# Optimization experiments

Hardware: AMD Instinct MI355X
Metric: run time of the kernel (lower is better)

Reference implementation:

```python
import jax, jax.numpy as jnp
import numpy as np

LN_EPS = 1e-5  # torch.nn.LayerNorm default


def setup_inputs() -> dict:
    key = jax.random.key(0)
    k1, k2, k3 = jax.random.split(key, 3)
    B, N, F, D = 8, 2048, 128, 128
    A_hat = jax.random.uniform(k1, (B, N, N), dtype=jnp.float32)
    X = jax.random.normal(k2, (B, N, F), dtype=jnp.float32)
    W = jax.random.normal(k3, (D, F), dtype=jnp.float32) * (1.0 / np.sqrt(F))
    b = jnp.zeros((D,), dtype=jnp.float32)
    gamma = jnp.ones((D,), dtype=jnp.float32)
    beta = jnp.zeros((D,), dtype=jnp.float32)
    return {"A_hat": A_hat, "X": X, "W": W, "b": b, "gamma": gamma, "beta": beta}


def reference(A_hat, X, W, b, gamma, beta):
    # batched aggregation: H[b] = A_hat[b] @ X[b]   (torch loop over batch, vectorized here)
    H = jnp.einsum('bnm,bmf->bnf', A_hat, X)
    # linear: torch nn.Linear stores W as [out, in]
    H = jnp.einsum('bnf,df->bnd', H, W) + b
    # LayerNorm over last dim, then ReLU (dropout p=0 -> identity)
    mu = jnp.mean(H, axis=-1, keepdims=True)
    var = jnp.mean((H - mu) ** 2, axis=-1, keepdims=True)
    Hn = (H - mu) * jax.lax.rsqrt(var + LN_EPS) * gamma + beta
    return jax.nn.relu(Hn)
```

## Files before the change

### kernel.cpp

```cpp
#include <hip/hip_runtime.h>
#include <stdint.h>

#define B_DIM 8
#define N_DIM 2048
#define F_DIM 128
#define LN_EPS 1e-5f

typedef __attribute__((ext_vector_type(8))) short short8;
typedef __attribute__((ext_vector_type(4))) float floatx4;

__device__ __forceinline__ ushort f2bf(float f) {
    union { float f; uint32_t u; } c;
    c.f = f;
    uint32_t u = c.u;
    return (ushort)((u + 0x7FFFu + ((u >> 16) & 1u)) >> 16);
}

__device__ __forceinline__ uint32_t pk2bf(float a, float b) {
    union { float f; uint32_t u; } x, y;
    x.f = a; y.f = b;
    return ((x.u + 0x8000u) >> 16) | ((y.u + 0x8000u) & 0xFFFF0000u);
}

__device__ __forceinline__ short8 pack8(float4 lo, float4 hi) {
    union { uint32_t u[4]; short8 s; } r;
    r.u[0] = pk2bf(lo.x, lo.y);
    r.u[1] = pk2bf(lo.z, lo.w);
    r.u[2] = pk2bf(hi.x, hi.y);
    r.u[3] = pk2bf(hi.z, hi.w);
    return r.s;
}

__device__ __forceinline__ void load_lds16(const ushort* g, ushort* l) {
    __builtin_amdgcn_global_load_lds(
        (const __attribute__((address_space(1))) void*)g,
        (__attribute__((address_space(3))) void*)l,
        16, 0, 0);
}

__global__ __launch_bounds__(256) void k_transpose(const float* __restrict__ X,
                                                   ushort* __restrict__ Xt) {
    __shared__ ushort tile[64 * 65];
    const int t = threadIdx.x;
    const int b = blockIdx.z;
    const int k0 = blockIdx.x * 64;
    const int f0 = blockIdx.y * 64;

#pragma unroll
    for (int p = 0; p < 2; ++p) {
        int idx = p * 256 + t;
        int kk = idx >> 3;
        int ff = (idx & 7) * 8;
        const float* src = X + (((size_t)b * N_DIM) + k0 + kk) * F_DIM + f0 + ff;
        float4 v0 = *(const float4*)(src);
        float4 v1 = *(const float4*)(src + 4);
        ushort* d = tile + kk * 65 + ff;
        d[0] = f2bf(v0.x); d[1] = f2bf(v0.y); d[2] = f2bf(v0.z); d[3] = f2bf(v0.w);
        d[4] = f2bf(v1.x); d[5] = f2bf(v1.y); d[6] = f2bf(v1.z); d[7] = f2bf(v1.w);
    }
    __syncthreads();

    union U { uint4 v; ushort s[8]; };
#pragma unroll
    for (int p = 0; p < 2; ++p) {
        int idx = p * 256 + t;
        int f2 = idx >> 3;
        int kk2 = (idx & 7) * 8;
        U u;
#pragma unroll
        for (int j = 0; j < 8; ++j) u.s[j] = tile[(kk2 + j) * 65 + f2];
        *(uint4*)(Xt + (((size_t)b * F_DIM) + f0 + f2) * N_DIM + k0 + kk2) = u.v;
    }
}

__global__ __launch_bounds__(256) void k_fused(const float* __restrict__ A,
                                               const ushort* __restrict__ Xt,
                                               const float* __restrict__ W,
                                               const float* __restrict__ bias,
                                               const float* __restrict__ gamma,
                                               const float* __restrict__ beta,
                                               float* __restrict__ out) {
    __shared__ __align__(16) ushort As[32 * 128];
    __shared__ __align__(16) ushort Bs[128 * 128];
    __shared__ __align__(16) ushort Ht[32 * 136];
    __shared__ float Pt[32][132];

    const int t = threadIdx.x;
    const int lane = t & 63;
    const int w = t >> 6;
    const int q = lane >> 4;
    const int mr = lane & 15;

    const int bid = blockIdx.x;
    const int bb = bid & 7;
    const int m0 = (bid >> 3) * 32;

    const float* Ab = A + ((size_t)bb * N_DIM + m0) * N_DIM;
    const ushort* Xb = Xt + (size_t)bb * F_DIM * N_DIM;

    const int arow = t >> 3;
    const int asw_ = arow & 7;
    const float* a_src = Ab + (size_t)arow * N_DIM + (t & 7) * 16;
    ushort* a_dst0 = As + arow * 128 + ((((t & 7) * 2) ^ asw_) * 8);
    ushort* a_dst1 = As + arow * 128 + ((((t & 7) * 2 + 1) ^ asw_) * 8);

    const ushort* b_src[8];
    ushort* b_dst[8];
#pragma unroll
    for (int p = 0; p < 8; ++p) {
        int c = p * 256 + t;
        int n = c >> 4;
        int kc = (c & 15) ^ (n & 7);
        b_src[p] = Xb + (size_t)n * N_DIM + kc * 8;
        b_dst[p] = Bs + c * 8;
    }

    floatx4 acc[2][2];
#pragma unroll
    for (int i = 0; i < 2; ++i)
#pragma unroll
        for (int j = 0; j < 2; ++j) acc[i][j] = (floatx4){0.f, 0.f, 0.f, 0.f};

    for (int k0 = 0; k0 < N_DIM; k0 += 128) {
        float4 v0 = ((const float4*)(a_src + k0))[0];
        float4 v1 = ((const float4*)(a_src + k0))[1];
        float4 v2 = ((const float4*)(a_src + k0))[2];
        float4 v3 = ((const float4*)(a_src + k0))[3];
#pragma unroll
        for (int p = 0; p < 8; ++p) load_lds16(b_src[p] + k0, b_dst[p]);
        *(short8*)a_dst0 = pack8(v0, v1);
        *(short8*)a_dst1 = pack8(v2, v3);
        __syncthreads();

#pragma unroll
        for (int ks = 0; ks < 4; ++ks) {
            short8 af[2], bf[2];
#pragma unroll
            for (int i = 0; i < 2; ++i) {
                int m = mr + i * 16;
                af[i] = *(const short8*)(As + m * 128 + (((ks * 4 + q) ^ (m & 7)) * 8));
            }
#pragma unroll
            for (int j = 0; j < 2; ++j) {
                int n = w * 32 + j * 16 + mr;
                bf[j] = *(const short8*)(Bs + n * 128 + (((ks * 4 + q) ^ (n & 7)) * 8));
            }
#pragma unroll
            for (int i = 0; i < 2; ++i)
#pragma unroll
                for (int j = 0; j < 2; ++j)
                    acc[i][j] = __builtin_amdgcn_mfma_f32_16x16x32_bf16(
                        af[i], bf[j], acc[i][j], 0, 0, 0);
        }
        __syncthreads();
    }

#pragma unroll
    for (int j = 0; j < 2; ++j) {
        int col = w * 32 + j * 16 + mr;
#pragma unroll
        for (int r = 0; r < 4; ++r) {
            Ht[(q * 4 + r) * 136 + col] = f2bf(acc[0][j][r]);
            Ht[(16 + q * 4 + r) * 136 + col] = f2bf(acc[1][j][r]);
        }
    }
    __syncthreads();

    floatx4 p[2][2];
#pragma unroll
    for (int i = 0; i < 2; ++i)
#pragma unroll
        for (int j = 0; j < 2; ++j) p[i][j] = (floatx4){0.f, 0.f, 0.f, 0.f};

#pragma unroll
    for (int ks = 0; ks < 4; ++ks) {
        short8 ha0 = *(const short8*)(Ht + mr * 136 + ks * 32 + q * 8);
        short8 ha1 = *(const short8*)(Ht + (mr + 16) * 136 + ks * 32 + q * 8);
#pragma unroll
        for (int j = 0; j < 2; ++j) {
            const float* wp = W + (w * 32 + j * 16 + mr) * F_DIM + ks * 32 + q * 8;
            short8 wb = pack8(((const float4*)wp)[0], ((const float4*)wp)[1]);
            p[0][j] = __builtin_amdgcn_mfma_f32_16x16x32_bf16(ha0, wb, p[0][j], 0, 0, 0);
            p[1][j] = __builtin_amdgcn_mfma_f32_16x16x32_bf16(ha1, wb, p[1][j], 0, 0, 0);
        }
    }

#pragma unroll
    for (int j = 0; j < 2; ++j) {
        int col = w * 32 + j * 16 + mr;
        float bcol = bias[col];
#pragma unroll
        for (int r = 0; r < 4; ++r) {
            Pt[q * 4 + r][col] = p[0][j][r] + bcol;
            Pt[16 + q * 4 + r][col] = p[1][j][r] + bcol;
        }
    }
    __syncthreads();

    const int row = t >> 3;
    const int seg = t & 7;
    float v[16];
    float s = 0.f, s2 = 0.f;
#pragma unroll
    for (int u = 0; u < 16; ++u) {
        v[u] = Pt[row][seg * 16 + u];
        s += v[u];
        s2 += v[u] * v[u];
    }
    s += __shfl_xor(s, 1);  s2 += __shfl_xor(s2, 1);
    s += __shfl_xor(s, 2);  s2 += __shfl_xor(s2, 2);
    s += __shfl_xor(s, 4);  s2 += __shfl_xor(s2, 4);
    float mu = s * (1.0f / 128.0f);
    float var = s2 * (1.0f / 128.0f) - mu * mu;
    float rs = rsqrtf(var + LN_EPS);

    float4 o[4];
    float* of = (float*)o;
#pragma unroll
    for (int u = 0; u < 16; ++u) {
        int d = seg * 16 + u;
        float y = (v[u] - mu) * rs * gamma[d] + beta[d];
        of[u] = fmaxf(y, 0.0f);
    }
    float4* dst = (float4*)(out + ((size_t)bb * N_DIM + m0 + row) * F_DIM + seg * 16);
    dst[0] = o[0]; dst[1] = o[1]; dst[2] = o[2]; dst[3] = o[3];
}

extern "C" void kernel_launch(void* const* d_in, const int* in_sizes, int n_in,
                              void* d_out, int out_size, void* d_ws, size_t ws_size,
                              hipStream_t stream) {
    const float* A     = (const float*)d_in[0];
    const float* X     = (const float*)d_in[1];
    const float* W     = (const float*)d_in[2];
    const float* bias  = (const float*)d_in[3];
    const float* gamma = (const float*)d_in[4];
    const float* beta  = (const float*)d_in[5];
    float* out = (float*)d_out;

    ushort* Xt = (ushort*)d_ws;

    k_transpose<<<dim3(32, 2, 8), 256, 0, stream>>>(X, Xt);
    k_fused<<<dim3(512), 256, 0, stream>>>(A, Xt, W, bias, gamma, beta, out);
}
```

Measured before the change: 214.3 us.

## Double-buffer A and B tiles with register prefetch in aggregation GEMM loop

Adds ping-pong LDS buffers for the A and Xt tiles and prefetches the next A tile into registers while the MFMAs run on the current one. Manual waitcnt/s_barrier replaces the two __syncthreads per iteration so global loads overlap compute. LDS grows to 80KB per block, reusing the buffers for the epilogue, which lowers occupancy. The hand-placed waitcnt counts add correctness risk if the compiler reorders loads.

Result: no change. 210.9 us (-1.6%).

```diff
diff --git a/kernel.cpp b/kernel.cpp
--- a/kernel.cpp
+++ b/kernel.cpp
@@ -80,10 +80,13 @@
                                                const float* __restrict__ gamma,
                                                const float* __restrict__ beta,
                                                float* __restrict__ out) {
-    __shared__ __align__(16) ushort As[32 * 128];
-    __shared__ __align__(16) ushort Bs[128 * 128];
-    __shared__ __align__(16) ushort Ht[32 * 136];
-    __shared__ float Pt[32][132];
+    __shared__ __align__(16) char smem[81920];
+    ushort* const As0 = (ushort*)smem;
+    ushort* const As1 = (ushort*)(smem + 8192);
+    ushort* const Bs0 = (ushort*)(smem + 16384);
+    ushort* const Bs1 = (ushort*)(smem + 16384 + 32768);
+    ushort* const Ht = (ushort*)smem;
+    float (*const Pt)[132] = (float(*)[132])(smem + 16384);
 
     const int t = threadIdx.x;
     const int lane = t & 63;
@@ -101,18 +104,18 @@
     const int arow = t >> 3;
     const int asw_ = arow & 7;
     const float* a_src = Ab + (size_t)arow * N_DIM + (t & 7) * 16;
-    ushort* a_dst0 = As + arow * 128 + ((((t & 7) * 2) ^ asw_) * 8);
-    ushort* a_dst1 = As + arow * 128 + ((((t & 7) * 2 + 1) ^ asw_) * 8);
+    const int a_off0 = arow * 128 + ((((t & 7) * 2) ^ asw_) * 8);
+    const int a_off1 = arow * 128 + ((((t & 7) * 2 + 1) ^ asw_) * 8);
 
     const ushort* b_src[8];
-    ushort* b_dst[8];
+    int b_off[8];
 #pragma unroll
     for (int p = 0; p < 8; ++p) {
         int c = p * 256 + t;
         int n = c >> 4;
         int kc = (c & 15) ^ (n & 7);
         b_src[p] = Xb + (size_t)n * N_DIM + kc * 8;
-        b_dst[p] = Bs + c * 8;
+        b_off[p] = c * 8;
     }
 
     floatx4 acc[2][2];
@@ -121,39 +124,85 @@
 #pragma unroll
         for (int j = 0; j < 2; ++j) acc[i][j] = (floatx4){0.f, 0.f, 0.f, 0.f};
 
-    for (int k0 = 0; k0 < N_DIM; k0 += 128) {
-        float4 v0 = ((const float4*)(a_src + k0))[0];
-        float4 v1 = ((const float4*)(a_src + k0))[1];
-        float4 v2 = ((const float4*)(a_src + k0))[2];
-        float4 v3 = ((const float4*)(a_src + k0))[3];
-#pragma unroll
-        for (int p = 0; p < 8; ++p) load_lds16(b_src[p] + k0, b_dst[p]);
-        *(short8*)a_dst0 = pack8(v0, v1);
-        *(short8*)a_dst1 = pack8(v2, v3);
-        __syncthreads();
-
+    auto stageB = [&](int k0, ushort* Bn) {
+#pragma unroll
+        for (int p = 0; p < 8; ++p) load_lds16(b_src[p] + k0, Bn + b_off[p]);
+    };
+    auto packA = [&](float4 v0, float4 v1, float4 v2, float4 v3, ushort* An) {
+        *(short8*)(An + a_off0) = pack8(v0, v1);
+        *(short8*)(An + a_off1) = pack8(v2, v3);
+    };
+    auto compute = [&](const ushort* Ac, const ushort* Bc) {
 #pragma unroll
         for (int ks = 0; ks < 4; ++ks) {
-            short8 af[2], bf[2];
+            short8 af[2], bfr[2];
 #pragma unroll
             for (int i = 0; i < 2; ++i) {
                 int m = mr + i * 16;
-                af[i] = *(const short8*)(As + m * 128 + (((ks * 4 + q) ^ (m & 7)) * 8));
+                af[i] = *(const short8*)(Ac + m * 128 + (((ks * 4 + q) ^ (m & 7)) * 8));
             }
 #pragma unroll
             for (int j = 0; j < 2; ++j) {
                 int n = w * 32 + j * 16 + mr;
-                bf[j] = *(const short8*)(Bs + n * 128 + (((ks * 4 + q) ^ (n & 7)) * 8));
+                bfr[j] = *(const short8*)(Bc + n * 128 + (((ks * 4 + q) ^ (n & 7)) * 8));
             }
 #pragma unroll
             for (int i = 0; i < 2; ++i)
 #pragma unroll
                 for (int j = 0; j < 2; ++j)
                     acc[i][j] = __builtin_amdgcn_mfma_f32_16x16x32_bf16(
-                        af[i], bf[j], acc[i][j], 0, 0, 0);
-        }
-        __syncthreads();
-    }
+                        af[i], bfr[j], acc[i][j], 0, 0, 0);
+        }
+    };
+
+    float4 r0a, r0b, r0c, r0d, r1a, r1b, r1c, r1d;
+
+    {
+        const float4* ap = (const float4*)(a_src);
+        r0a = ap[0]; r0b = ap[1]; r0c = ap[2]; r0d = ap[3];
+        stageB(0, Bs0);
+        packA(r0a, r0b, r0c, r0d, As0);
+        __builtin_amdgcn_sched_barrier(0);
+        const float4* ap1 = (const float4*)(a_src + 128);
+        r1a = ap1[0]; r1b = ap1[1]; r1c = ap1[2]; r1d = ap1[3];
+    }
+    asm volatile("s_waitcnt vmcnt(4) lgkmcnt(0)" ::: "memory");
+    __builtin_amdgcn_s_barrier();
+
+#pragma unroll 1
+    for (int tt = 0; tt < 14; tt += 2) {
+        const int k0 = tt * 128;
+        stageB(k0 + 128, Bs1);
+        __builtin_amdgcn_sched_barrier(0);
+        {
+            const float4* ap = (const float4*)(a_src + k0 + 256);
+            r0a = ap[0]; r0b = ap[1]; r0c = ap[2]; r0d = ap[3];
+        }
+        compute(As0, Bs0);
+        packA(r1a, r1b, r1c, r1d, As1);
+        asm volatile("s_waitcnt vmcnt(4) lgkmcnt(0)" ::: "memory");
+        __builtin_amdgcn_s_barrier();
+
+        stageB(k0 + 256, Bs0);
+        __builtin_amdgcn_sched_barrier(0);
+        {
+            const float4* ap = (const float4*)(a_src + k0 + 384);
+            r1a = ap[0]; r1b = ap[1]; r1c = ap[2]; r1d = ap[3];
+        }
+        compute(As1, Bs1);
+        packA(r0a, r0b, r0c, r0d, As0);
+        asm volatile("s_waitcnt vmcnt(4) lgkmcnt(0)" ::: "memory");
+        __builtin_amdgcn_s_barrier();
+    }
+
+    stageB(15 * 128, Bs1);
+    compute(As0, Bs0);
+    packA(r1a, r1b, r1c, r1d, As1);
+    asm volatile("s_waitcnt vmcnt(0) lgkmcnt(0)" ::: "memory");
+    __builtin_amdgcn_s_barrier();
+
+    compute(As1, Bs1);
+    __syncthreads();
 
 #pragma unroll
     for (int j = 0; j < 2; ++j) {
```

## Fuse X conversion into main kernel with double-buffered register-prefetch pipeline

Applied to the files above, without the earlier changes.

Drops the separate transpose kernel. The fused kernel now loads fp32 X directly, converts it to bf16 and stores it swizzled in LDS, then gathers the B fragments with strided scalar LDS reads. The K loop uses a 64-wide tile with double-buffered LDS and register prefetch of the next tile, so there is one barrier per step instead of two. It also sets launch bounds to 3 blocks per CU. The cost is that every block re-reads and re-converts fp32 X (64 blocks per batch), and the LDS gathers for B are scalar 16-bit reads, which may be slow.

Result: slower. 235.1 us (+9.7%).

```diff
diff --git a/kernel.cpp b/kernel.cpp
--- a/kernel.cpp
+++ b/kernel.cpp
@@ -31,59 +31,20 @@
     return r.s;
 }
 
-__device__ __forceinline__ void load_lds16(const ushort* g, ushort* l) {
-    __builtin_amdgcn_global_load_lds(
-        (const __attribute__((address_space(1))) void*)g,
-        (__attribute__((address_space(3))) void*)l,
-        16, 0, 0);
-}
-
-__global__ __launch_bounds__(256) void k_transpose(const float* __restrict__ X,
-                                                   ushort* __restrict__ Xt) {
-    __shared__ ushort tile[64 * 65];
-    const int t = threadIdx.x;
-    const int b = blockIdx.z;
-    const int k0 = blockIdx.x * 64;
-    const int f0 = blockIdx.y * 64;
-
-#pragma unroll
-    for (int p = 0; p < 2; ++p) {
-        int idx = p * 256 + t;
-        int kk = idx >> 3;
-        int ff = (idx & 7) * 8;
-        const float* src = X + (((size_t)b * N_DIM) + k0 + kk) * F_DIM + f0 + ff;
-        float4 v0 = *(const float4*)(src);
-        float4 v1 = *(const float4*)(src + 4);
-        ushort* d = tile + kk * 65 + ff;
-        d[0] = f2bf(v0.x); d[1] = f2bf(v0.y); d[2] = f2bf(v0.z); d[3] = f2bf(v0.w);
-        d[4] = f2bf(v1.x); d[5] = f2bf(v1.y); d[6] = f2bf(v1.z); d[7] = f2bf(v1.w);
-    }
-    __syncthreads();
-
-    union U { uint4 v; ushort s[8]; };
-#pragma unroll
-    for (int p = 0; p < 2; ++p) {
-        int idx = p * 256 + t;
-        int f2 = idx >> 3;
-        int kk2 = (idx & 7) * 8;
-        U u;
-#pragma unroll
-        for (int j = 0; j < 8; ++j) u.s[j] = tile[(kk2 + j) * 65 + f2];
-        *(uint4*)(Xt + (((size_t)b * F_DIM) + f0 + f2) * N_DIM + k0 + kk2) = u.v;
-    }
-}
-
-__global__ __launch_bounds__(256) void k_fused(const float* __restrict__ A,
-                                               const ushort* __restrict__ Xt,
-                                               const float* __restrict__ W,
-                                               const float* __restrict__ bias,
-                                               const float* __restrict__ gamma,
-                                               const float* __restrict__ beta,
-                                               float* __restrict__ out) {
-    __shared__ __align__(16) ushort As[32 * 128];
-    __shared__ __align__(16) ushort Bs[128 * 128];
-    __shared__ __align__(16) ushort Ht[32 * 136];
-    __shared__ float Pt[32][132];
+__global__ __launch_bounds__(256, 3) void k_fused(const float* __restrict__ A,
+                                                  const float* __restrict__ X,
+                                                  const float* __restrict__ W,
+                                                  const float* __restrict__ bias,
+                                                  const float* __restrict__ gamma,
+                                                  const float* __restrict__ beta,
+                                                  float* __restrict__ out) {
+    __shared__ __align__(16) char smem[43008];
+    ushort* const As0 = (ushort*)smem;
+    ushort* const As1 = (ushort*)(smem + 4096);
+    ushort* const Xs0 = (ushort*)(smem + 8192);
+    ushort* const Xs1 = (ushort*)(smem + 25600);
+    ushort* const Ht = (ushort*)smem;
+    float (*const Pt)[132] = (float(*)[132])(smem + 9216);
 
     const int t = threadIdx.x;
     const int lane = t & 63;
@@ -96,24 +57,23 @@
     const int m0 = (bid >> 3) * 32;
 
     const float* Ab = A + ((size_t)bb * N_DIM + m0) * N_DIM;
-    const ushort* Xb = Xt + (size_t)bb * F_DIM * N_DIM;
-
-    const int arow = t >> 3;
-    const int asw_ = arow & 7;
-    const float* a_src = Ab + (size_t)arow * N_DIM + (t & 7) * 16;
-    ushort* a_dst0 = As + arow * 128 + ((((t & 7) * 2) ^ asw_) * 8);
-    ushort* a_dst1 = As + arow * 128 + ((((t & 7) * 2 + 1) ^ asw_) * 8);
-
-    const ushort* b_src[8];
-    ushort* b_dst[8];
-#pragma unroll
-    for (int p = 0; p < 8; ++p) {
-        int c = p * 256 + t;
-        int n = c >> 4;
-        int kc = (c & 15) ^ (n & 7);
-        b_src[p] = Xb + (size_t)n * N_DIM + kc * 8;
-        b_dst[p] = Bs + c * 8;
-    }
+    const float* Xb = X + (size_t)bb * N_DIM * F_DIM;
+
+    const int ar = t >> 3;
+    const int ac = t & 7;
+    const float* a_src = Ab + (size_t)ar * N_DIM + ac * 8;
+    const int a_off = ar * 64 + ((ac ^ (ar & 7)) * 8);
+
+    const int xr = t >> 3;
+    const int xc = (t & 7) * 16;
+    const float* x_base0 = Xb + (size_t)xr * F_DIM + xc;
+    const float* x_base1 = Xb + (size_t)(32 + xr) * F_DIM + xc;
+    const int key0 = xr >> 3;
+    const int key1 = 4 + (xr >> 3);
+    const int xoff0 = xr * 136 + (((xc >> 3) ^ key0) * 8);
+    const int xoff1 = xr * 136 + ((((xc >> 3) + 1) ^ key0) * 8);
+    const int xoff2 = (32 + xr) * 136 + (((xc >> 3) ^ key1) * 8);
+    const int xoff3 = (32 + xr) * 136 + ((((xc >> 3) + 1) ^ key1) * 8);
 
     floatx4 acc[2][2];
 #pragma unroll
@@ -121,39 +81,78 @@
 #pragma unroll
         for (int j = 0; j < 2; ++j) acc[i][j] = (floatx4){0.f, 0.f, 0.f, 0.f};
 
-    for (int k0 = 0; k0 < N_DIM; k0 += 128) {
-        float4 v0 = ((const float4*)(a_src + k0))[0];
-        float4 v1 = ((const float4*)(a_src + k0))[1];
-        float4 v2 = ((const float4*)(a_src + k0))[2];
-        float4 v3 = ((const float4*)(a_src + k0))[3];
-#pragma unroll
-        for (int p = 0; p < 8; ++p) load_lds16(b_src[p] + k0, b_dst[p]);
-        *(short8*)a_dst0 = pack8(v0, v1);
-        *(short8*)a_dst1 = pack8(v2, v3);
-        __syncthreads();
-
-#pragma unroll
-        for (int ks = 0; ks < 4; ++ks) {
-            short8 af[2], bf[2];
+    float4 X0a[4], X0b[4], A0v[2];
+    float4 X1a[4], X1b[4], A1v[2];
+
+    auto issue = [&](int k0, float4* Xa, float4* Xc, float4* Av) {
+        const float4* p0 = (const float4*)(x_base0 + (size_t)k0 * F_DIM);
+        Xa[0] = p0[0]; Xa[1] = p0[1]; Xa[2] = p0[2]; Xa[3] = p0[3];
+        const float4* p1 = (const float4*)(x_base1 + (size_t)k0 * F_DIM);
+        Xc[0] = p1[0]; Xc[1] = p1[1]; Xc[2] = p1[2]; Xc[3] = p1[3];
+        const float4* pa = (const float4*)(a_src + k0);
+        Av[0] = pa[0]; Av[1] = pa[1];
+    };
+    auto packT = [&](const float4* Xa, const float4* Xc, const float4* Av,
+                     ushort* Xs_, ushort* As_) {
+        *(short8*)(Xs_ + xoff0) = pack8(Xa[0], Xa[1]);
+        *(short8*)(Xs_ + xoff1) = pack8(Xa[2], Xa[3]);
+        *(short8*)(Xs_ + xoff2) = pack8(Xc[0], Xc[1]);
+        *(short8*)(Xs_ + xoff3) = pack8(Xc[2], Xc[3]);
+        *(short8*)(As_ + a_off) = pack8(Av[0], Av[1]);
+    };
+    auto compute = [&](const ushort* Ac, const ushort* Xc) {
+#pragma unroll
+        for (int ks = 0; ks < 2; ++ks) {
+            short8 af[2];
 #pragma unroll
             for (int i = 0; i < 2; ++i) {
                 int m = mr + i * 16;
-                af[i] = *(const short8*)(As + m * 128 + (((ks * 4 + q) ^ (m & 7)) * 8));
+                af[i] = *(const short8*)(Ac + m * 64 +
+                                         (((ks * 4 + q) ^ (m & 7)) * 8));
             }
 #pragma unroll
             for (int j = 0; j < 2; ++j) {
                 int n = w * 32 + j * 16 + mr;
-                bf[j] = *(const short8*)(Bs + n * 128 + (((ks * 4 + q) ^ (n & 7)) * 8));
+                union { ushort s[8]; short8 v; } u;
+#pragma unroll
+                for (int r = 0; r < 8; ++r)
+                    u.s[r] = Xc[(ks * 32 + q * 8 + r) * 136 +
+                                (((n >> 3) ^ (ks * 4 + q)) * 8) + (n & 7)];
+                acc[0][j] = __builtin_amdgcn_mfma_f32_16x16x32_bf16(
+                    af[0], u.v, acc[0][j], 0, 0, 0);
+                acc[1][j] = __builtin_amdgcn_mfma_f32_16x16x32_bf16(
+                    af[1], u.v, acc[1][j], 0, 0, 0);
             }
-#pragma unroll
-            for (int i = 0; i < 2; ++i)
-#pragma unroll
-                for (int j = 0; j < 2; ++j)
-                    acc[i][j] = __builtin_amdgcn_mfma_f32_16x16x32_bf16(
-                        af[i], bf[j], acc[i][j], 0, 0, 0);
-        }
-        __syncthreads();
-    }
+        }
+    };
+
+    issue(0, X0a, X0b, A0v);
+    packT(X0a, X0b, A0v, Xs0, As0);
+    issue(64, X1a, X1b, A1v);
+    asm volatile("s_waitcnt lgkmcnt(0)" ::: "memory");
+    __builtin_amdgcn_s_barrier();
+
+#pragma unroll 1
+    for (int tt = 0; tt < 30; tt += 2) {
+        compute(As0, Xs0);
+        packT(X1a, X1b, A1v, Xs1, As1);
+        issue((tt + 2) * 64, X0a, X0b, A0v);
+        asm volatile("s_waitcnt lgkmcnt(0)" ::: "memory");
+        __builtin_amdgcn_s_barrier();
+
+        compute(As1, Xs1);
+        packT(X0a, X0b, A0v, Xs0, As0);
+        issue((tt + 3) * 64, X1a, X1b, A1v);
+        asm volatile("s_waitcnt lgkmcnt(0)" ::: "memory");
+        __builtin_amdgcn_s_barrier();
+    }
+
+    compute(As0, Xs0);
+    packT(X1a, X1b, A1v, Xs1, As1);
+    asm volatile("s_waitcnt lgkmcnt(0)" ::: "memory");
+    __builtin_amdgcn_s_barrier();
+    compute(As1, Xs1);
+    __syncthreads();
 
 #pragma unroll
     for (int j = 0; j < 2; ++j) {
@@ -237,8 +236,7 @@
     const float* beta  = (const float*)d_in[5];
     float* out = (float*)d_out;
 
-    ushort* Xt = (ushort*)d_ws;
-
-    k_transpose<<<dim3(32, 2, 8), 256, 0, stream>>>(X, Xt);
-    k_fused<<<dim3(512), 256, 0, stream>>>(A, Xt, W, bias, gamma, beta, out);
-}
+    (void)d_ws; (void)ws_size;
+
+    k_fused<<<dim3(512), 256, 0, stream>>>(A, X, W, bias, gamma, beta, out);
+}
```
